# Kernel optimization log

Hardware: AMD Instinct MI355X
Metric: run time of the kernel (lower is better)

## Reference

```python
import jax, jax.numpy as jnp
import numpy as np

H = 256
V = 50257
L = 2048
B = 32


def setup_inputs() -> dict:
    key = jax.random.key(0)
    ks = jax.random.split(key, 14)
    s = 0.05  # weight scale
    return {
        "tokens": jax.random.randint(ks[0], (B,), 0, V),
        "hidden": jax.random.normal(ks[1], (1, B, H), jnp.float32),
        "cell": jax.random.normal(ks[2], (1, B, H), jnp.float32),
        "encoder_outputs": jax.random.normal(ks[3], (B, L, H), jnp.float32),
        "emb_table": jax.random.normal(ks[4], (V, H), jnp.float32) * s,
        "W_attn": jax.random.normal(ks[5], (H, 2 * H), jnp.float32) * s,
        "b_attn": jax.random.normal(ks[6], (H,), jnp.float32) * s,
        "v": jax.random.normal(ks[7], (H,), jnp.float32) * s,
        "W_ih": jax.random.normal(ks[8], (4 * H, 2 * H), jnp.float32) * s,
        "b_ih": jax.random.normal(ks[9], (4 * H,), jnp.float32) * s,
        "W_hh": jax.random.normal(ks[10], (4 * H, H), jnp.float32) * s,
        "b_hh": jax.random.normal(ks[11], (4 * H,), jnp.float32) * s,
        "W_out": jax.random.normal(ks[12], (V, 2 * H), jnp.float32) * s,
        "b_out": jax.random.normal(ks[13], (V,), jnp.float32) * s,
    }


def reference(tokens, hidden, cell, encoder_outputs, emb_table, W_attn, b_attn, v,
              W_ih, b_ih, W_hh, b_hh, W_out, b_out):
    # embedded: (B, H); dropout is identity in eval mode
    embedded = emb_table[tokens]
    h_last = hidden[-1]  # (B, H)

    # Bahdanau-style energy: attn(cat(h, e)) then dot with v (NO tanh, per source)
    # split the 2H-input linear into hidden part and encoder part
    Wh, We = W_attn[:, :H], W_attn[:, H:]
    eh = h_last @ Wh.T                                      # (B, H)
    ee = jnp.einsum('blh,kh->blk', encoder_outputs, We)     # (B, L, H)
    energy = eh[:, None, :] + ee + b_attn                   # (B, L, H)
    scores = energy @ v                                     # (B, L)
    attn_weights = jax.nn.softmax(scores, axis=-1)          # (B, L)

    # context = bmm(attn_weights, encoder_outputs)
    attn_applied = jnp.einsum('bl,blh->bh', attn_weights, encoder_outputs)  # (B, H)

    # single-step LSTM, input = cat(embedded, context): (B, 2H)
    x = jnp.concatenate([embedded, attn_applied], axis=-1)
    gates = x @ W_ih.T + b_ih + hidden[0] @ W_hh.T + b_hh   # (B, 4H)
    i_g, f_g, g_g, o_g = jnp.split(gates, 4, axis=-1)
    c_new = jax.nn.sigmoid(f_g) * cell[0] + jax.nn.sigmoid(i_g) * jnp.tanh(g_g)
    h_new = jax.nn.sigmoid(o_g) * jnp.tanh(c_new)           # (B, H)

    # output projection on cat(lstm_out, context): (B, 2H) -> (B, V)
    logits = jnp.concatenate([h_new, attn_applied], axis=-1) @ W_out.T + b_out
    log_probs = jax.nn.log_softmax(logits, axis=-1)

    return (log_probs, h_new[None], c_new[None], attn_weights[:, None, :])
```

## Files before the change

### kernel.cpp

```cpp
#include <hip/hip_runtime.h>
#include <cstddef>

#define H   256
#define L   2048
#define B   32
#define V   50257
#define H2  512
#define H4  1024

#define LP_OFF 0
#define HN_OFF (B*V)
#define CN_OFF (HN_OFF + B*H)
#define AW_OFF (CN_OFF + B*H)

#define WS_W     0
#define WS_XG    256
#define WS_XL    (WS_XG + B*H2)
#define WS_PART  (WS_XL + B*H2)
#define WS_PM    WS_PART
#define WS_PZ    (WS_PM + 12800)
#define WS_GATES (WS_PART + B*16*H)
#define WS_M     (WS_GATES + B*H4)
#define WS_LZ    (WS_M + 32)

#define NBLK_LOG 393

typedef __attribute__((ext_vector_type(8))) short bf16x8;
typedef __attribute__((ext_vector_type(4))) float f32x4;

__device__ inline unsigned short f2bf(float f) {
    unsigned u = __builtin_bit_cast(unsigned, f);
    u += 0x7FFFu + ((u >> 16) & 1u);
    return (unsigned short)(u >> 16);
}

__global__ __launch_bounds__(1024) void k_prep(const float* __restrict__ W_attn, const float* __restrict__ v,
                                               const int* __restrict__ tokens, const float* __restrict__ emb,
                                               float* __restrict__ ws) {
    int t = threadIdx.x;
    if (blockIdx.x == 0) {
        __shared__ float wred[4 * 256];
        int kq = t >> 8;
        int h  = t & 255;
        const float* base = W_attn + H + h;
        float acc = 0.f;
        #pragma unroll 8
        for (int k = kq * 64; k < kq * 64 + 64; k++) acc += v[k] * base[(size_t)k * H2];
        wred[kq * 256 + h] = acc;
        __syncthreads();
        if (t < 256) {
            ws[WS_W + t] = wred[t] + wred[256 + t] + wred[512 + t] + wred[768 + t];
        }
    } else if (t < 256) {
        int b = blockIdx.x - 1;
        int tok = tokens[b];
        ws[WS_XG + b * H2 + t] = emb[(size_t)tok * H + t];
    }
}

__global__ __launch_bounds__(256) void k_scores(const float* __restrict__ enc,
                                                const float* __restrict__ ws,
                                                float* __restrict__ out) {
    int t = threadIdx.x;
    int wave = t >> 6, lane = t & 63;
    int id = blockIdx.x * 4 + wave;
    const float4* e4 = (const float4*)(enc + (size_t)id * H);
    const float4* w4 = (const float4*)(ws + WS_W);
    float4 a = e4[lane];
    float4 w = w4[lane];
    float p = a.x * w.x + a.y * w.y + a.z * w.z + a.w * w.w;
    #pragma unroll
    for (int off = 32; off; off >>= 1) p += __shfl_down(p, off);
    if (lane == 0) out[AW_OFF + id] = p;
}

__global__ __launch_bounds__(256) void k_attn_softmax(float* __restrict__ out) {
    int b = blockIdx.x, t = threadIdx.x;
    __shared__ float red[256];
    float* s = out + AW_OFF + (size_t)b * L;
    float vals[8];
    float vmax = -1e30f;
    #pragma unroll
    for (int j = 0; j < 8; j++) { vals[j] = s[t + 256 * j]; vmax = fmaxf(vmax, vals[j]); }
    red[t] = vmax; __syncthreads();
    for (int off = 128; off; off >>= 1) { if (t < off) red[t] = fmaxf(red[t], red[t + off]); __syncthreads(); }
    float m = red[0]; __syncthreads();
    float sum = 0.f;
    #pragma unroll
    for (int j = 0; j < 8; j++) { vals[j] = expf(vals[j] - m); sum += vals[j]; }
    red[t] = sum; __syncthreads();
    for (int off = 128; off; off >>= 1) { if (t < off) red[t] += red[t + off]; __syncthreads(); }
    float inv = 1.f / red[0];
    #pragma unroll
    for (int j = 0; j < 8; j++) s[t + 256 * j] = vals[j] * inv;
}

__global__ __launch_bounds__(256) void k_attn_partial(const float* __restrict__ enc,
                                                      const float* __restrict__ out,
                                                      float* __restrict__ ws) {
    int bid = blockIdx.x;
    int b = bid >> 4, chunk = bid & 15;
    int t = threadIdx.x;
    __shared__ float wgt[128];
    if (t < 128) wgt[t] = out[AW_OFF + (size_t)b * L + chunk * 128 + t];
    __syncthreads();
    const float* e = enc + ((size_t)b * L + chunk * 128) * H + t;
    float acc = 0.f;
    #pragma unroll 4
    for (int l = 0; l < 128; l++) acc += wgt[l] * e[(size_t)l * H];
    ws[WS_PART + (size_t)bid * H + t] = acc;
}

__global__ __launch_bounds__(256) void k_attn_reduce(float* __restrict__ ws) {
    int b = blockIdx.x, t = threadIdx.x;
    float acc = 0.f;
    #pragma unroll
    for (int c = 0; c < 16; c++) acc += ws[WS_PART + (size_t)(b * 16 + c) * H + t];
    ws[WS_XG + b * H2 + H + t] = acc;
    ws[WS_XL + b * H2 + H + t] = acc;
}

__global__ __launch_bounds__(256) void k_gates(const float* __restrict__ W_ih, const float* __restrict__ b_ih,
                                               const float* __restrict__ W_hh, const float* __restrict__ b_hh,
                                               const float* __restrict__ hidden, float* __restrict__ ws) {
    int t = threadIdx.x;
    int wave = t >> 6, lane = t & 63;
    int o = blockIdx.x * 4 + wave;
    int b = o >> 10, j = o & 1023;
    const float4* wi = (const float4*)(W_ih + (size_t)j * H2);
    const float4* xg = (const float4*)(ws + WS_XG + (size_t)b * H2);
    float4 a0 = wi[lane * 2], a1 = wi[lane * 2 + 1];
    float4 x0 = xg[lane * 2], x1 = xg[lane * 2 + 1];
    float p = a0.x * x0.x + a0.y * x0.y + a0.z * x0.z + a0.w * x0.w
            + a1.x * x1.x + a1.y * x1.y + a1.z * x1.z + a1.w * x1.w;
    const float4* wh = (const float4*)(W_hh + (size_t)j * H);
    const float4* hp = (const float4*)(hidden + (size_t)b * H);
    float4 a2 = wh[lane], x2 = hp[lane];
    p += a2.x * x2.x + a2.y * x2.y + a2.z * x2.z + a2.w * x2.w;
    #pragma unroll
    for (int off = 32; off; off >>= 1) p += __shfl_down(p, off);
    if (lane == 0) ws[WS_GATES + o] = p + b_ih[j] + b_hh[j];
}

__global__ __launch_bounds__(256) void k_lstm(const float* __restrict__ cell,
                                              float* __restrict__ ws, float* __restrict__ out) {
    int b = blockIdx.x, t = threadIdx.x;
    const float* g = ws + WS_GATES + (size_t)b * H4;
    float ig = g[t], fg = g[H + t], gg = g[2 * H + t], og = g[3 * H + t];
    float c = cell[(size_t)b * H + t];
    float si = 1.f / (1.f + expf(-ig));
    float sf = 1.f / (1.f + expf(-fg));
    float so = 1.f / (1.f + expf(-og));
    float cn = sf * c + si * tanhf(gg);
    float hn = so * tanhf(cn);
    out[HN_OFF + b * H + t] = hn;
    out[CN_OFF + b * H + t] = cn;
    ws[WS_XL + b * H2 + t] = hn;
}

__global__ __launch_bounds__(256) void k_logits(const float* __restrict__ W_out,
                                                const float* __restrict__ b_out,
                                                float* __restrict__ ws,
                                                float* __restrict__ out) {
    __shared__ unsigned short Xl[32 * 520];
    int t = threadIdx.x;
    const float4* xl4 = (const float4*)(ws + WS_XL);
    #pragma unroll
    for (int it = 0; it < 16; it++) {
        int fi = t + 256 * it;
        int b = fi >> 7, kq = fi & 127;
        float4 xv = xl4[b * 128 + kq];
        unsigned p0 = (unsigned)f2bf(xv.x) | ((unsigned)f2bf(xv.y) << 16);
        unsigned p1 = (unsigned)f2bf(xv.z) | ((unsigned)f2bf(xv.w) << 16);
        unsigned* dst = (unsigned*)&Xl[b * 520 + kq * 4];
        dst[0] = p0; dst[1] = p1;
    }
    __syncthreads();

    int wave = t >> 6, lane = t & 63, quad = lane >> 4, m = lane & 15;
    int rbase = blockIdx.x * 128 + wave * 32;
    f32x4 zero4 = {0.f, 0.f, 0.f, 0.f};
    f32x4 acc[2][2];
    acc[0][0] = zero4; acc[0][1] = zero4; acc[1][0] = zero4; acc[1][1] = zero4;

    int r0 = rbase + m;
    int r1 = rbase + 16 + m;
    bool v0 = r0 < V, v1 = r1 < V;
    const float* wp0 = W_out + (size_t)r0 * H2 + quad * 8;
    const float* wp1 = W_out + (size_t)r1 * H2 + quad * 8;

    for (int kp = 0; kp < 16; kp++) {
        int k0 = kp * 32;
        bf16x8 a0 = {0,0,0,0,0,0,0,0}, a1 = {0,0,0,0,0,0,0,0};
        if (v0) {
            float4 lo = *(const float4*)(wp0 + k0);
            float4 hi = *(const float4*)(wp0 + k0 + 4);
            a0[0]=(short)f2bf(lo.x); a0[1]=(short)f2bf(lo.y); a0[2]=(short)f2bf(lo.z); a0[3]=(short)f2bf(lo.w);
            a0[4]=(short)f2bf(hi.x); a0[5]=(short)f2bf(hi.y); a0[6]=(short)f2bf(hi.z); a0[7]=(short)f2bf(hi.w);
        }
        if (v1) {
            float4 lo = *(const float4*)(wp1 + k0);
            float4 hi = *(const float4*)(wp1 + k0 + 4);
            a1[0]=(short)f2bf(lo.x); a1[1]=(short)f2bf(lo.y); a1[2]=(short)f2bf(lo.z); a1[3]=(short)f2bf(lo.w);
            a1[4]=(short)f2bf(hi.x); a1[5]=(short)f2bf(hi.y); a1[6]=(short)f2bf(hi.z); a1[7]=(short)f2bf(hi.w);
        }
        bf16x8 b0 = *(bf16x8*)&Xl[(size_t)m * 520 + k0 + quad * 8];
        bf16x8 b1 = *(bf16x8*)&Xl[(size_t)(16 + m) * 520 + k0 + quad * 8];
        acc[0][0] = __builtin_amdgcn_mfma_f32_16x16x32_bf16(a0, b0, acc[0][0], 0, 0, 0);
        acc[0][1] = __builtin_amdgcn_mfma_f32_16x16x32_bf16(a0, b1, acc[0][1], 0, 0, 0);
        acc[1][0] = __builtin_amdgcn_mfma_f32_16x16x32_bf16(a1, b0, acc[1][0], 0, 0, 0);
        acc[1][1] = __builtin_amdgcn_mfma_f32_16x16x32_bf16(a1, b1, acc[1][1], 0, 0, 0);
    }

    float val[2][2][4];
    #pragma unroll
    for (int s = 0; s < 2; s++) {
        #pragma unroll
        for (int i = 0; i < 4; i++) {
            int rr = rbase + s * 16 + quad * 4 + i;
            float bo = (rr < V) ? b_out[rr] : 0.f;
            #pragma unroll
            for (int nt = 0; nt < 2; nt++) {
                float vv = acc[s][nt][i] + bo;
                if (rr < V) {
                    int bcol = nt * 16 + m;
                    out[(size_t)bcol * V + rr] = vv;
                    val[s][nt][i] = vv;
                } else {
                    val[s][nt][i] = -1e30f;
                }
            }
        }
    }
    float pm[2], pz[2];
    #pragma unroll
    for (int nt = 0; nt < 2; nt++) {
        float mx = -1e30f;
        #pragma unroll
        for (int s = 0; s < 2; s++)
            #pragma unroll
            for (int i = 0; i < 4; i++) mx = fmaxf(mx, val[s][nt][i]);
        float sm = 0.f;
        #pragma unroll
        for (int s = 0; s < 2; s++)
            #pragma unroll
            for (int i = 0; i < 4; i++) sm += __expf(val[s][nt][i] - mx);
        pm[nt] = mx; pz[nt] = sm;
    }
    #pragma unroll
    for (int off = 16; off <= 32; off <<= 1) {
        #pragma unroll
        for (int nt = 0; nt < 2; nt++) {
            float om = __shfl_xor(pm[nt], off);
            float oz = __shfl_xor(pz[nt], off);
            float nm = fmaxf(pm[nt], om);
            pz[nt] = pz[nt] * __expf(pm[nt] - nm) + oz * __expf(om - nm);
            pm[nt] = nm;
        }
    }
    __syncthreads();
    float* red = (float*)Xl;
    if (quad == 0) {
        #pragma unroll
        for (int nt = 0; nt < 2; nt++) {
            red[wave * 32 + nt * 16 + m]       = pm[nt];
            red[128 + wave * 32 + nt * 16 + m] = pz[nt];
        }
    }
    __syncthreads();
    if (t < 32) {
        float mf = -1e30f;
        #pragma unroll
        for (int w = 0; w < 4; w++) mf = fmaxf(mf, red[w * 32 + t]);
        float z = 0.f;
        #pragma unroll
        for (int w = 0; w < 4; w++) z += red[128 + w * 32 + t] * __expf(red[w * 32 + t] - mf);
        ws[WS_PM + t * 400 + blockIdx.x] = mf;
        ws[WS_PZ + t * 400 + blockIdx.x] = z;
    }
}

__global__ __launch_bounds__(256) void k_lsm_comb(float* __restrict__ ws) {
    int b = blockIdx.x, t = threadIdx.x;
    float m = -1e30f, z = 0.f;
    for (int i = t; i < NBLK_LOG; i += 256) {
        float mi = ws[WS_PM + b * 400 + i];
        float zi = ws[WS_PZ + b * 400 + i];
        float nm = fmaxf(m, mi);
        z = z * __expf(m - nm) + zi * __expf(mi - nm);
        m = nm;
    }
    __shared__ float rm[256], rz[256];
    rm[t] = m; rz[t] = z; __syncthreads();
    for (int off = 128; off; off >>= 1) {
        if (t < off) {
            float m2 = rm[t + off], z2 = rz[t + off];
            float nm = fmaxf(rm[t], m2);
            rz[t] = rz[t] * __expf(rm[t] - nm) + z2 * __expf(m2 - nm);
            rm[t] = nm;
        }
        __syncthreads();
    }
    if (t == 0) { ws[WS_M + b] = rm[0]; ws[WS_LZ + b] = logf(rz[0]); }
}

__global__ __launch_bounds__(256) void k_lsm_final(const float* __restrict__ ws, float* __restrict__ out) {
    int b = blockIdx.y;
    int r = blockIdx.x * 256 + threadIdx.x;
    if (r < V) {
        size_t i = (size_t)b * V + r;
        out[i] = out[i] - ws[WS_M + b] - ws[WS_LZ + b];
    }
}

extern "C" void kernel_launch(void* const* d_in, const int* in_sizes, int n_in,
                              void* d_out, int out_size, void* d_ws, size_t ws_size,
                              hipStream_t stream) {
    const int*   tokens = (const int*)d_in[0];
    const float* hidden = (const float*)d_in[1];
    const float* cell   = (const float*)d_in[2];
    const float* enc    = (const float*)d_in[3];
    const float* emb    = (const float*)d_in[4];
    const float* W_attn = (const float*)d_in[5];
    const float* v      = (const float*)d_in[7];
    const float* W_ih   = (const float*)d_in[8];
    const float* b_ih   = (const float*)d_in[9];
    const float* W_hh   = (const float*)d_in[10];
    const float* b_hh   = (const float*)d_in[11];
    const float* W_out  = (const float*)d_in[12];
    const float* b_out  = (const float*)d_in[13];
    float* out = (float*)d_out;
    float* ws  = (float*)d_ws;

    k_prep<<<1 + B, 1024, 0, stream>>>(W_attn, v, tokens, emb, ws);
    k_scores<<<(B * L) / 4, 256, 0, stream>>>(enc, ws, out);
    k_attn_softmax<<<B, 256, 0, stream>>>(out);
    k_attn_partial<<<B * 16, 256, 0, stream>>>(enc, out, ws);
    k_attn_reduce<<<B, 256, 0, stream>>>(ws);
    k_gates<<<(B * H4) / 4, 256, 0, stream>>>(W_ih, b_ih, W_hh, b_hh, hidden, ws);
    k_lstm<<<B, 256, 0, stream>>>(cell, ws, out);
    k_logits<<<NBLK_LOG, 256, 0, stream>>>(W_out, b_out, ws, out);
    k_lsm_comb<<<B, 256, 0, stream>>>(ws);
    k_lsm_final<<<dim3((V + 255) / 256, B), 256, 0, stream>>>(ws, out);
}
```

Baseline: 296.5 us.

## Fuse attention scores, softmax and context into flash-style chunked kernel

Replaces the separate score, softmax, partial-context and reduce kernels with one kernel per (batch, chunk) that computes scores, a local max/sum and an unnormalized weighted sum of the encoder rows. A small combine kernel then merges the chunk results with online-softmax rescaling, writes the normalized attention weights, and also does the embedding gather. The aim is to read the 64MB encoder tensor once from a chunk that stays cache-resident instead of twice, and to cut kernel launches. In exchange the score pass is serialized within each wave over 32 rows, and the extra workspace traffic for scores is small.

```diff
diff --git a/kernel.cpp b/kernel.cpp
--- a/kernel.cpp
+++ b/kernel.cpp
@@ -16,11 +16,14 @@
 #define WS_W     0
 #define WS_XG    256
 #define WS_XL    (WS_XG + B*H2)
-#define WS_PART  (WS_XL + B*H2)
-#define WS_PM    WS_PART
+#define WS_S     (WS_XL + B*H2)
+#define WS_AV    (WS_S + B*L)
+#define WS_AM    (WS_AV + 512*256)
+#define WS_AZ    (WS_AM + 512)
+#define WS_GATES (WS_AZ + 512)
+#define WS_PM    (WS_GATES + B*H4)
 #define WS_PZ    (WS_PM + 12800)
-#define WS_GATES (WS_PART + B*16*H)
-#define WS_M     (WS_GATES + B*H4)
+#define WS_M     (WS_PZ + 12800)
 #define WS_LZ    (WS_M + 32)
 
 #define NBLK_LOG 393
@@ -34,90 +37,98 @@
     return (unsigned short)(u >> 16);
 }
 
-__global__ __launch_bounds__(1024) void k_prep(const float* __restrict__ W_attn, const float* __restrict__ v,
-                                               const int* __restrict__ tokens, const float* __restrict__ emb,
+__global__ __launch_bounds__(1024) void k_prep(const float* __restrict__ W_attn,
+                                               const float* __restrict__ v,
                                                float* __restrict__ ws) {
+    __shared__ float wred[1024];
     int t = threadIdx.x;
-    if (blockIdx.x == 0) {
-        __shared__ float wred[4 * 256];
-        int kq = t >> 8;
-        int h  = t & 255;
-        const float* base = W_attn + H + h;
-        float acc = 0.f;
-        #pragma unroll 8
-        for (int k = kq * 64; k < kq * 64 + 64; k++) acc += v[k] * base[(size_t)k * H2];
-        wred[kq * 256 + h] = acc;
-        __syncthreads();
-        if (t < 256) {
-            ws[WS_W + t] = wred[t] + wred[256 + t] + wred[512 + t] + wred[768 + t];
-        }
-    } else if (t < 256) {
-        int b = blockIdx.x - 1;
-        int tok = tokens[b];
-        ws[WS_XG + b * H2 + t] = emb[(size_t)tok * H + t];
-    }
-}
-
-__global__ __launch_bounds__(256) void k_scores(const float* __restrict__ enc,
-                                                const float* __restrict__ ws,
-                                                float* __restrict__ out) {
-    int t = threadIdx.x;
-    int wave = t >> 6, lane = t & 63;
-    int id = blockIdx.x * 4 + wave;
-    const float4* e4 = (const float4*)(enc + (size_t)id * H);
-    const float4* w4 = (const float4*)(ws + WS_W);
-    float4 a = e4[lane];
-    float4 w = w4[lane];
-    float p = a.x * w.x + a.y * w.y + a.z * w.z + a.w * w.w;
-    #pragma unroll
-    for (int off = 32; off; off >>= 1) p += __shfl_down(p, off);
-    if (lane == 0) out[AW_OFF + id] = p;
-}
-
-__global__ __launch_bounds__(256) void k_attn_softmax(float* __restrict__ out) {
-    int b = blockIdx.x, t = threadIdx.x;
-    __shared__ float red[256];
-    float* s = out + AW_OFF + (size_t)b * L;
-    float vals[8];
-    float vmax = -1e30f;
-    #pragma unroll
-    for (int j = 0; j < 8; j++) { vals[j] = s[t + 256 * j]; vmax = fmaxf(vmax, vals[j]); }
-    red[t] = vmax; __syncthreads();
-    for (int off = 128; off; off >>= 1) { if (t < off) red[t] = fmaxf(red[t], red[t + off]); __syncthreads(); }
-    float m = red[0]; __syncthreads();
-    float sum = 0.f;
-    #pragma unroll
-    for (int j = 0; j < 8; j++) { vals[j] = expf(vals[j] - m); sum += vals[j]; }
-    red[t] = sum; __syncthreads();
-    for (int off = 128; off; off >>= 1) { if (t < off) red[t] += red[t + off]; __syncthreads(); }
-    float inv = 1.f / red[0];
-    #pragma unroll
-    for (int j = 0; j < 8; j++) s[t + 256 * j] = vals[j] * inv;
-}
-
-__global__ __launch_bounds__(256) void k_attn_partial(const float* __restrict__ enc,
-                                                      const float* __restrict__ out,
-                                                      float* __restrict__ ws) {
+    int kq = t >> 8;
+    int h  = t & 255;
+    const float* base = W_attn + H + h;
+    float acc = 0.f;
+    #pragma unroll 16
+    for (int k = kq * 64; k < kq * 64 + 64; k++) acc += v[k] * base[(size_t)k * H2];
+    wred[t] = acc;
+    __syncthreads();
+    if (t < 256) ws[WS_W + t] = wred[t] + wred[256 + t] + wred[512 + t] + wred[768 + t];
+}
+
+__global__ __launch_bounds__(256) void k_attn_flash(const float* __restrict__ enc,
+                                                    float* __restrict__ ws) {
     int bid = blockIdx.x;
     int b = bid >> 4, chunk = bid & 15;
     int t = threadIdx.x;
-    __shared__ float wgt[128];
-    if (t < 128) wgt[t] = out[AW_OFF + (size_t)b * L + chunk * 128 + t];
-    __syncthreads();
-    const float* e = enc + ((size_t)b * L + chunk * 128) * H + t;
+    int wave = t >> 6, lane = t & 63;
+    __shared__ float s_lds[128];
+    __shared__ float p_lds[128];
+    __shared__ float red[128];
+    __shared__ float vec_lds[4][256];
+
+    const float4* w4p = (const float4*)(ws + WS_W);
+    float4 wv = w4p[lane];
+    size_t rowbase = (size_t)b * L + chunk * 128;
+
+    for (int i = 0; i < 32; i++) {
+        int l = wave * 32 + i;
+        const float4* e4 = (const float4*)(enc + (rowbase + l) * H);
+        float4 a = e4[lane];
+        float p = a.x * wv.x + a.y * wv.y + a.z * wv.z + a.w * wv.w;
+        #pragma unroll
+        for (int off = 32; off; off >>= 1) p += __shfl_down(p, off);
+        if (lane == 0) s_lds[l] = p;
+    }
+    __syncthreads();
+    if (t < 128) { ws[WS_S + rowbase + t] = s_lds[t]; red[t] = s_lds[t]; }
+    __syncthreads();
+    for (int off = 64; off; off >>= 1) { if (t < off) red[t] = fmaxf(red[t], red[t + off]); __syncthreads(); }
+    float m = red[0];
+    __syncthreads();
+    if (t < 128) { float e = __expf(s_lds[t] - m); p_lds[t] = e; red[t] = e; }
+    __syncthreads();
+    for (int off = 64; off; off >>= 1) { if (t < off) red[t] += red[t + off]; __syncthreads(); }
+
+    float4 acc = make_float4(0.f, 0.f, 0.f, 0.f);
+    const float4* ebase = (const float4*)(enc + (rowbase + wave * 32) * H);
+    #pragma unroll 4
+    for (int i = 0; i < 32; i++) {
+        float p = p_lds[wave * 32 + i];
+        float4 a = ebase[i * 64 + lane];
+        acc.x += p * a.x; acc.y += p * a.y; acc.z += p * a.z; acc.w += p * a.w;
+    }
+    *(float4*)&vec_lds[wave][lane * 4] = acc;
+    __syncthreads();
+    ws[WS_AV + (size_t)bid * 256 + t] = vec_lds[0][t] + vec_lds[1][t] + vec_lds[2][t] + vec_lds[3][t];
+    if (t == 0) { ws[WS_AM + bid] = m; ws[WS_AZ + bid] = red[0]; }
+}
+
+__global__ __launch_bounds__(256) void k_attn_comb(const int* __restrict__ tokens,
+                                                   const float* __restrict__ emb,
+                                                   float* __restrict__ ws,
+                                                   float* __restrict__ out) {
+    int b = blockIdx.x, t = threadIdx.x;
+    __shared__ float mc[16], zc[16];
+    if (t < 16) { mc[t] = ws[WS_AM + b * 16 + t]; zc[t] = ws[WS_AZ + b * 16 + t]; }
+    __syncthreads();
+    float M = -1e30f;
+    #pragma unroll
+    for (int c = 0; c < 16; c++) M = fmaxf(M, mc[c]);
+    float Z = 0.f;
+    #pragma unroll
+    for (int c = 0; c < 16; c++) Z += zc[c] * __expf(mc[c] - M);
+    float inv = 1.f / Z;
     float acc = 0.f;
-    #pragma unroll 4
-    for (int l = 0; l < 128; l++) acc += wgt[l] * e[(size_t)l * H];
-    ws[WS_PART + (size_t)bid * H + t] = acc;
-}
-
-__global__ __launch_bounds__(256) void k_attn_reduce(float* __restrict__ ws) {
-    int b = blockIdx.x, t = threadIdx.x;
-    float acc = 0.f;
-    #pragma unroll
-    for (int c = 0; c < 16; c++) acc += ws[WS_PART + (size_t)(b * 16 + c) * H + t];
+    #pragma unroll
+    for (int c = 0; c < 16; c++) acc += __expf(mc[c] - M) * ws[WS_AV + (size_t)(b * 16 + c) * 256 + t];
+    acc *= inv;
     ws[WS_XG + b * H2 + H + t] = acc;
     ws[WS_XL + b * H2 + H + t] = acc;
+    int tok = tokens[b];
+    ws[WS_XG + b * H2 + t] = emb[(size_t)tok * H + t];
+    #pragma unroll
+    for (int j = 0; j < 8; j++) {
+        int l = t + 256 * j;
+        out[AW_OFF + (size_t)b * L + l] = __expf(ws[WS_S + (size_t)b * L + l] - M) * inv;
+    }
 }
 
 __global__ __launch_bounds__(256) void k_gates(const float* __restrict__ W_ih, const float* __restrict__ b_ih,
@@ -332,11 +343,9 @@
     float* out = (float*)d_out;
     float* ws  = (float*)d_ws;
 
-    k_prep<<<1 + B, 1024, 0, stream>>>(W_attn, v, tokens, emb, ws);
-    k_scores<<<(B * L) / 4, 256, 0, stream>>>(enc, ws, out);
-    k_attn_softmax<<<B, 256, 0, stream>>>(out);
-    k_attn_partial<<<B * 16, 256, 0, stream>>>(enc, out, ws);
-    k_attn_reduce<<<B, 256, 0, stream>>>(ws);
+    k_prep<<<1, 1024, 0, stream>>>(W_attn, v, ws);
+    k_attn_flash<<<B * 16, 256, 0, stream>>>(enc, ws);
+    k_attn_comb<<<B, 256, 0, stream>>>(tokens, emb, ws, out);
     k_gates<<<(B * H4) / 4, 256, 0, stream>>>(W_ih, b_ih, W_hh, b_hh, hidden, ws);
     k_lstm<<<B, 256, 0, stream>>>(cell, ws, out);
     k_logits<<<NBLK_LOG, 256, 0, stream>>>(W_out, b_out, ws, out);
```

New measurement: 302.5 us. 2.0% more time.
